# Kernel tuning notes

Hardware: AMD Instinct MI355X
Metric: run time of the kernel (lower is better)

Reference implementation:

```python
import jax, jax.numpy as jnp
import numpy as np

B, S, D = 2, 2048, 1024
E, K = 8, 2
CAP_FACTOR = 1.25
HID = 4 * D


def _capacity(num_tokens: int) -> int:
    import math
    cap = math.floor(K * CAP_FACTOR * num_tokens / E)
    cap += cap % 2
    return max(int(cap), 2)


def setup_inputs() -> dict:
    key = jax.random.key(0)
    k1, k2, k3, k4 = jax.random.split(key, 4)
    x = jax.random.normal(k1, (B, S, D), dtype=jnp.float32)
    w_gate = jax.random.normal(k2, (D, E), dtype=jnp.float32) * 0.02
    w_fc = jax.random.normal(k3, (E, D, HID), dtype=jnp.float32) * 0.02
    w_proj = jax.random.normal(k4, (E, HID, D), dtype=jnp.float32) * 0.02
    return {"x": x, "w_gate": w_gate, "w_fc": w_fc, "w_proj": w_proj}


def _moe_forward(x, w_gate, w_fc, w_proj):
    b, s, d = x.shape
    T = b * s
    cap = _capacity(T)
    xf = x.astype(jnp.float32).reshape(T, d)

    # --- Router (fp32, eval mode: no noise) ---
    logits = xf @ w_gate                                   # [T, E]
    top_v, top_i = jax.lax.top_k(logits, K)                # [T, K]
    NEG = jnp.float32(-1e30)
    masked = jnp.full_like(logits, NEG)
    masked = masked.at[jnp.arange(T)[:, None], top_i].set(top_v)
    probs = jax.nn.softmax(masked, axis=-1)                # [T, E], zero off top-k

    # --- Capacity assignment: cumsum over (k-major, token) flattened order ---
    oh = jax.nn.one_hot(top_i, E, dtype=jnp.int32)         # [T, K, E]
    oh = jnp.transpose(oh, (1, 0, 2))                      # [K, T, E]
    rank = jnp.cumsum(oh.reshape(K * T, E), axis=0).reshape(K, T, E) - 1
    within = (oh > 0) & (rank < cap)                       # [K, T, E]
    rank_sel = jnp.sum(jnp.where(within, rank, 0), axis=-1)  # [K, T]
    kept = jnp.any(within, axis=-1)                        # [K, T]

    p = jnp.take_along_axis(probs, top_i, axis=-1).T       # [K, T]
    w = jnp.where(kept, p, 0.0)                            # combine weights

    e_idx = top_i.T                                        # [K, T]
    t_idx = jnp.broadcast_to(jnp.arange(T)[None, :], (K, T))

    # expert_weights[t, e, c] (sparse scatter == torch one-hot combine)
    expert_weights = jnp.zeros((T, E, cap), jnp.float32)
    expert_weights = expert_weights.at[t_idx.ravel(), e_idx.ravel(), rank_sel.ravel()].add(w.ravel())

    # dispatch: expert_batches[e, c, :] = x of token routed to (e, c)
    disp = jnp.where(kept, 1.0, 0.0).ravel()[:, None]      # [K*T, 1]
    expert_batches = jnp.zeros((E, cap, d), jnp.float32)
    expert_batches = expert_batches.at[e_idx.ravel(), rank_sel.ravel()].add(disp * xf[t_idx.ravel()])

    # --- Expert MLPs (batched GEMMs, exact GELU, no bias, eval dropout) ---
    h = jnp.einsum('ecd,edh->ech', expert_batches, w_fc)
    h = jax.nn.gelu(h, approximate=False)
    expert_out = jnp.einsum('ech,ehd->ecd', h, w_proj)      # [E, cap, d]

    # --- Combine: gather expert outputs back to tokens weighted by router prob ---
    gathered = expert_out[e_idx.ravel(), rank_sel.ravel()].reshape(K, T, d)
    out_flat = jnp.sum(w[:, :, None] * gathered, axis=0)    # [T, d]
    output = out_flat.reshape(b, s, d)

    # --- Load balance loss (Switch) ---
    probs_full = jax.nn.softmax(logits, axis=-1)
    prob_per_expert = jnp.mean(probs_full, axis=0)          # [E]
    tokens_per_expert = jax.lax.stop_gradient(
        jnp.sum((expert_weights > 0).astype(jnp.float32), axis=(0, 2)) / (T * K)
    )
    lb_loss = E * jnp.sum(prob_per_expert * tokens_per_expert)

    # --- Router z-loss ---
    z_loss = jnp.mean(jax.nn.logsumexp(logits, axis=-1) ** 2)
    return output, lb_loss, z_loss


def reference(x, w_gate, w_fc, w_proj):
    return _moe_forward(x, w_gate, w_fc, w_proj)
```

## Files before the change

### kernel.cpp

```cpp
#include <hip/hip_runtime.h>
#include <hip/hip_bf16.h>
#include <cstdint>
#include <cstddef>

#define T_TOK 4096
#define D_DIM 1024
#define E_EXP 8
#define KSEL 2
#define CAP 1280
#define HID_DIM 4096

typedef __attribute__((ext_vector_type(8))) __bf16 bf16x8;
typedef __attribute__((ext_vector_type(8))) unsigned short ushort8;
typedef __attribute__((ext_vector_type(4))) float floatx4;

__device__ __forceinline__ unsigned short f2bf(float f) {
  unsigned int u = __builtin_bit_cast(unsigned int, f);
  u = (u + 0x7FFFu + ((u >> 16) & 1u)) >> 16;
  return (unsigned short)u;
}
__device__ __forceinline__ float bf2f(unsigned short h) {
  unsigned int u = ((unsigned int)h) << 16;
  return __builtin_bit_cast(float, u);
}

__device__ __forceinline__ void async16(const unsigned short* g, unsigned short* l) {
  __builtin_amdgcn_global_load_lds(
      (const __attribute__((address_space(1))) unsigned int*)g,
      (__attribute__((address_space(3))) unsigned int*)l, 16, 0, 0);
}

__global__ void router_kernel(const float* __restrict__ x, const float* __restrict__ wg,
                              int* __restrict__ top1, int* __restrict__ top2,
                              float* __restrict__ p0, float* __restrict__ p1,
                              float* __restrict__ probsum, float* __restrict__ zsum) {
  __shared__ float lps[E_EXP];
  __shared__ float lz;
  if (threadIdx.x < E_EXP) lps[threadIdx.x] = 0.f;
  if (threadIdx.x == 0) lz = 0.f;
  __syncthreads();
  int wave = threadIdx.x >> 6;
  int lane = threadIdx.x & 63;
  int t = blockIdx.x * 4 + wave;
  const float* xr = x + (size_t)t * D_DIM;
  float acc[E_EXP];
#pragma unroll
  for (int e = 0; e < E_EXP; ++e) acc[e] = 0.f;
  for (int j = 0; j < D_DIM / 64; ++j) {
    int i = lane + 64 * j;
    float xv = xr[i];
    const float4* wr = (const float4*)(wg + (size_t)i * E_EXP);
    float4 w0 = wr[0], w1 = wr[1];
    acc[0] += xv * w0.x; acc[1] += xv * w0.y; acc[2] += xv * w0.z; acc[3] += xv * w0.w;
    acc[4] += xv * w1.x; acc[5] += xv * w1.y; acc[6] += xv * w1.z; acc[7] += xv * w1.w;
  }
#pragma unroll
  for (int e = 0; e < E_EXP; ++e) {
#pragma unroll
    for (int s = 32; s > 0; s >>= 1) acc[e] += __shfl_xor(acc[e], s);
  }
  if (lane == 0) {
    int i1 = 0; float v1 = acc[0];
    for (int e = 1; e < E_EXP; ++e) if (acc[e] > v1) { v1 = acc[e]; i1 = e; }
    int i2 = -1; float v2 = -1e30f;
    for (int e = 0; e < E_EXP; ++e) if (e != i1 && acc[e] > v2) { v2 = acc[e]; i2 = e; }
    top1[t] = i1; top2[t] = i2;
    float dexp = expf(v2 - v1);
    p0[t] = 1.f / (1.f + dexp);
    p1[t] = dexp / (1.f + dexp);
    float pe[E_EXP]; float ssum = 0.f;
    for (int e = 0; e < E_EXP; ++e) { pe[e] = expf(acc[e] - v1); ssum += pe[e]; }
    float lse = logf(ssum) + v1;
    atomicAdd(&lz, lse * lse);
    float inv = 1.f / ssum;
    for (int e = 0; e < E_EXP; ++e) atomicAdd(&lps[e], pe[e] * inv);
  }
  __syncthreads();
  if (threadIdx.x < E_EXP) atomicAdd(&probsum[threadIdx.x], lps[threadIdx.x]);
  if (threadIdx.x == 0) atomicAdd(zsum, lz);
}

__global__ void scan_kernel(const int* __restrict__ top1, const int* __restrict__ top2,
                            int* __restrict__ rank0, int* __restrict__ rank1,
                            int* __restrict__ slot_token, int* __restrict__ cntk) {
  __shared__ int sc[256][E_EXP];
  int c = threadIdx.x;
  int e0l[16], e1l[16];
  int c0[E_EXP], c1[E_EXP];
#pragma unroll
  for (int e = 0; e < E_EXP; ++e) { c0[e] = 0; c1[e] = 0; }
#pragma unroll
  for (int j = 0; j < 16; ++j) {
    int t = c * 16 + j;
    int a = top1[t]; int b = top2[t];
    e0l[j] = a; e1l[j] = b;
    c0[a]++; c1[b]++;
  }
  for (int e = 0; e < E_EXP; ++e) sc[c][e] = c0[e];
  __syncthreads();
  for (int s = 1; s < 256; s <<= 1) {
    int tmp[E_EXP];
    if (c >= s) { for (int e = 0; e < E_EXP; ++e) tmp[e] = sc[c - s][e]; }
    __syncthreads();
    if (c >= s) { for (int e = 0; e < E_EXP; ++e) sc[c][e] += tmp[e]; }
    __syncthreads();
  }
  int off0[E_EXP], tot0[E_EXP];
  for (int e = 0; e < E_EXP; ++e) {
    off0[e] = (c > 0) ? sc[c - 1][e] : 0;
    tot0[e] = sc[255][e];
  }
  __syncthreads();
  for (int e = 0; e < E_EXP; ++e) sc[c][e] = c1[e];
  __syncthreads();
  for (int s = 1; s < 256; s <<= 1) {
    int tmp[E_EXP];
    if (c >= s) { for (int e = 0; e < E_EXP; ++e) tmp[e] = sc[c - s][e]; }
    __syncthreads();
    if (c >= s) { for (int e = 0; e < E_EXP; ++e) sc[c][e] += tmp[e]; }
    __syncthreads();
  }
  int off1[E_EXP], tot1[E_EXP];
  for (int e = 0; e < E_EXP; ++e) {
    off1[e] = (c > 0) ? sc[c - 1][e] : 0;
    tot1[e] = sc[255][e];
  }
  int run[E_EXP];
  for (int e = 0; e < E_EXP; ++e) run[e] = off0[e];
#pragma unroll
  for (int j = 0; j < 16; ++j) {
    int t = c * 16 + j;
    int e = e0l[j];
    int r = run[e]++;
    if (r < CAP) { rank0[t] = r; slot_token[e * CAP + r] = t; } else rank0[t] = -1;
  }
  for (int e = 0; e < E_EXP; ++e) run[e] = tot0[e] + off1[e];
#pragma unroll
  for (int j = 0; j < 16; ++j) {
    int t = c * 16 + j;
    int e = e1l[j];
    int r = run[e]++;
    if (r < CAP) { rank1[t] = r; slot_token[e * CAP + r] = t; } else rank1[t] = -1;
  }
  if (c == 0) {
    for (int e = 0; e < E_EXP; ++e) {
      int tot = tot0[e] + tot1[e];
      cntk[e] = tot < CAP ? tot : CAP;
    }
  }
}

__global__ void dispatch_kernel(const float* __restrict__ x, const int* __restrict__ slot_token,
                                unsigned short* __restrict__ batch) {
  int slot = blockIdx.x;
  int t = slot_token[slot];
  int d = threadIdx.x * 4;
  ushort4 o;
  if (t >= 0) {
    float4 v = *(const float4*)(x + (size_t)t * D_DIM + d);
    o.x = f2bf(v.x); o.y = f2bf(v.y); o.z = f2bf(v.z); o.w = f2bf(v.w);
  } else {
    o.x = 0; o.y = 0; o.z = 0; o.w = 0;
  }
  *(ushort4*)(batch + (size_t)slot * D_DIM + d) = o;
}

__global__ __launch_bounds__(256) void transpose_convert(const float* __restrict__ in,
                                                         unsigned short* __restrict__ out,
                                                         int R, int C) {
  __shared__ float tile[64][65];
  int b = blockIdx.z;
  int c0 = blockIdx.x * 64;
  int r0 = blockIdx.y * 64;
  const float* ip = in + (size_t)b * R * C;
  unsigned short* op = out + (size_t)b * R * C;
  int tid = threadIdx.x;
  int rr = tid >> 4;
  int cc = (tid & 15) * 4;
#pragma unroll
  for (int it = 0; it < 4; ++it) {
    int r = rr + it * 16;
    float4 v = *(const float4*)(ip + (size_t)(r0 + r) * C + c0 + cc);
    tile[r][cc] = v.x; tile[r][cc + 1] = v.y; tile[r][cc + 2] = v.z; tile[r][cc + 3] = v.w;
  }
  __syncthreads();
  int c = tid >> 2;
  int rq = (tid & 3) * 16;
  unsigned short vals[16];
#pragma unroll
  for (int j = 0; j < 16; ++j) vals[j] = f2bf(tile[rq + j][c]);
  unsigned short* dst = op + (size_t)(c0 + c) * R + r0 + rq;
  *(ushort8*)dst = *(ushort8*)&vals[0];
  *(ushort8*)(dst + 8) = *(ushort8*)&vals[8];
}

template <int KD, int NN, int NG_TILES, bool GELU>
__global__ __launch_bounds__(256) void gemm_alds(const unsigned short* __restrict__ A,
                                                 const unsigned short* __restrict__ BT,
                                                 unsigned short* __restrict__ Cd,
                                                 const int* __restrict__ cntk) {
  constexpr int MT = CAP / 128;
  constexpr int GRP = MT * NG_TILES;
  int bid = blockIdx.x;
  int e = bid & 7;
  int slot = bid >> 3;
  int ng = slot / GRP;
  int rem = slot - ng * GRP;
  int mm = rem / NG_TILES;
  int nw = rem - mm * NG_TILES;
  int m0 = mm * 128;
  int n0 = (ng * NG_TILES + nw) * 128;
  if (m0 >= cntk[e]) return;
  const unsigned short* Ae = A + (size_t)e * CAP * KD;
  const unsigned short* Be = BT + (size_t)e * NN * KD;
  unsigned short* Ce = Cd + (size_t)e * CAP * NN;
  __shared__ unsigned short As[128 * 32];
  __shared__ unsigned short Bs[128 * 32];
  int tid = threadIdx.x;
  int lane = tid & 63;
  int wv = tid >> 6;
  int wm = (wv & 1) * 64;
  int wn = (wv >> 1) * 64;
  int mrow = lane & 15;
  int kqb = lane >> 4;
  int sx = (mrow >> 1) & 3;
  int kb = (kqb ^ sx) * 8;
  floatx4 acc[4][4];
#pragma unroll
  for (int i = 0; i < 4; ++i)
#pragma unroll
    for (int j = 0; j < 4; ++j) {
      floatx4 z = {0.f, 0.f, 0.f, 0.f};
      acc[i][j] = z;
    }
  for (int k0 = 0; k0 < KD; k0 += 32) {
#pragma unroll
    for (int i = 0; i < 2; ++i) {
      int chw = i * 256 + wv * 64;
      int ch = chw + lane;
      int r = ch >> 2;
      int cbs = (ch & 3) ^ ((r >> 1) & 3);
      async16(&Ae[(size_t)(m0 + r) * KD + k0 + cbs * 8], &As[chw * 8]);
      async16(&Be[(size_t)(n0 + r) * KD + k0 + cbs * 8], &Bs[chw * 8]);
    }
    __syncthreads();
    bf16x8 af[4], bfr[4];
#pragma unroll
    for (int mt = 0; mt < 4; ++mt)
      af[mt] = *(const bf16x8*)(&As[(wm + mt * 16 + mrow) * 32 + kb]);
#pragma unroll
    for (int nt = 0; nt < 4; ++nt)
      bfr[nt] = *(const bf16x8*)(&Bs[(wn + nt * 16 + mrow) * 32 + kb]);
#pragma unroll
    for (int mt = 0; mt < 4; ++mt)
#pragma unroll
      for (int nt = 0; nt < 4; ++nt)
        acc[mt][nt] = __builtin_amdgcn_mfma_f32_16x16x32_bf16(af[mt], bfr[nt], acc[mt][nt], 0, 0, 0);
    __syncthreads();
  }
  int crow = (lane >> 4) * 4;
  int ccol = lane & 15;
#pragma unroll
  for (int mt = 0; mt < 4; ++mt)
#pragma unroll
    for (int nt = 0; nt < 4; ++nt)
#pragma unroll
      for (int r = 0; r < 4; ++r) {
        float v = acc[mt][nt][r];
        if (GELU) v = 0.5f * v * (1.f + erff(v * 0.70710678118654752f));
        Ce[(size_t)(m0 + wm + mt * 16 + crow + r) * NN + (n0 + wn + nt * 16 + ccol)] = f2bf(v);
      }
}

__global__ void combine_kernel(const unsigned short* __restrict__ EO,
                               const int* __restrict__ top1, const int* __restrict__ top2,
                               const float* __restrict__ p0, const float* __restrict__ p1,
                               const int* __restrict__ rank0, const int* __restrict__ rank1,
                               float* __restrict__ out) {
  int t = blockIdx.x;
  int d = threadIdx.x * 4;
  float a0 = 0.f, a1 = 0.f, a2 = 0.f, a3 = 0.f;
  int r0 = rank0[t];
  if (r0 >= 0) {
    float w = p0[t];
    ushort4 v = *(const ushort4*)(EO + ((size_t)top1[t] * CAP + r0) * D_DIM + d);
    a0 += w * bf2f(v.x); a1 += w * bf2f(v.y); a2 += w * bf2f(v.z); a3 += w * bf2f(v.w);
  }
  int r1 = rank1[t];
  if (r1 >= 0) {
    float w = p1[t];
    ushort4 v = *(const ushort4*)(EO + ((size_t)top2[t] * CAP + r1) * D_DIM + d);
    a0 += w * bf2f(v.x); a1 += w * bf2f(v.y); a2 += w * bf2f(v.z); a3 += w * bf2f(v.w);
  }
  float4 o; o.x = a0; o.y = a1; o.z = a2; o.w = a3;
  *(float4*)(out + (size_t)t * D_DIM + d) = o;
}

__global__ void finalize_kernel(const float* __restrict__ probsum, const float* __restrict__ zsum,
                                const int* __restrict__ cntk, float* __restrict__ out) {
  if (threadIdx.x == 0) {
    float lb = 0.f;
    for (int e = 0; e < E_EXP; ++e)
      lb += (probsum[e] / (float)T_TOK) * ((float)cntk[e] / (float)(T_TOK * KSEL));
    out[(size_t)T_TOK * D_DIM] = lb * (float)E_EXP;
    out[(size_t)T_TOK * D_DIM + 1] = zsum[0] / (float)T_TOK;
  }
}

extern "C" void kernel_launch(void* const* d_in, const int* in_sizes, int n_in,
                              void* d_out, int out_size, void* d_ws, size_t ws_size,
                              hipStream_t stream) {
  const float* x = (const float*)d_in[0];
  const float* w_gate = (const float*)d_in[1];
  const float* w_fc = (const float*)d_in[2];
  const float* w_proj = (const float*)d_in[3];
  float* out = (float*)d_out;
  char* ws = (char*)d_ws;

  float* probsum = (float*)(ws + 0);
  float* zsum    = (float*)(ws + 32);
  int*   cntk    = (int*)(ws + 64);
  int*   top1    = (int*)(ws + 4096);
  int*   top2    = (int*)(ws + 20480);
  float* p0      = (float*)(ws + 36864);
  float* p1      = (float*)(ws + 53248);
  int*   rank0   = (int*)(ws + 69632);
  int*   rank1   = (int*)(ws + 86016);
  int*   slot    = (int*)(ws + 102400);
  unsigned short* batch = (unsigned short*)(ws + 262144);
  unsigned short* H     = (unsigned short*)(ws + 262144 + 20971520);
  unsigned short* EO    = (unsigned short*)(ws + 262144 + 20971520 + 83886080);
  unsigned short* W     = (unsigned short*)(ws + 262144 + 20971520 + 83886080 + 20971520);

  hipMemsetAsync(ws, 0, 4096, stream);
  hipMemsetAsync(slot, 0xFF, E_EXP * CAP * sizeof(int), stream);

  router_kernel<<<T_TOK / 4, 256, 0, stream>>>(x, w_gate, top1, top2, p0, p1, probsum, zsum);
  scan_kernel<<<1, 256, 0, stream>>>(top1, top2, rank0, rank1, slot, cntk);
  dispatch_kernel<<<E_EXP * CAP, 256, 0, stream>>>(x, slot, batch);

  transpose_convert<<<dim3(HID_DIM / 64, D_DIM / 64, E_EXP), 256, 0, stream>>>(w_fc, W, D_DIM, HID_DIM);
  gemm_alds<D_DIM, HID_DIM, 4, true><<<8 * (HID_DIM / 128 / 4) * (CAP / 128) * 4, 256, 0, stream>>>(batch, W, H, cntk);

  transpose_convert<<<dim3(D_DIM / 64, HID_DIM / 64, E_EXP), 256, 0, stream>>>(w_proj, W, HID_DIM, D_DIM);
  gemm_alds<HID_DIM, D_DIM, 2, false><<<8 * (D_DIM / 128 / 2) * (CAP / 128) * 2, 256, 0, stream>>>(H, W, EO, cntk);

  combine_kernel<<<T_TOK, 256, 0, stream>>>(EO, top1, top2, p0, p1, rank0, rank1, out);
  finalize_kernel<<<1, 64, 0, stream>>>(probsum, zsum, cntk, out);
}
```

Before: 584.1 us.

## Fuse fp32 weight conversion and transpose into expert GEMM B-tile loads

Removes the separate transpose_convert passes that produced bf16 transposed weight copies, and instead has each GEMM block load fp32 weights directly, convert to bf16 in registers, and write a transposed tile into padded LDS. Also merges the finalize kernel into the combine kernel. This saves the extra weight read/write pass and two launches, but doubles per-block weight bytes fetched and replaces async global-to-LDS loads for B with synchronous loads, which may expose latency.

```diff
diff --git a/kernel.cpp b/kernel.cpp
--- a/kernel.cpp
+++ b/kernel.cpp
@@ -12,6 +12,7 @@
 
 typedef __attribute__((ext_vector_type(8))) __bf16 bf16x8;
 typedef __attribute__((ext_vector_type(8))) unsigned short ushort8;
+typedef __attribute__((ext_vector_type(4))) unsigned short ushort4v;
 typedef __attribute__((ext_vector_type(4))) float floatx4;
 
 __device__ __forceinline__ unsigned short f2bf(float f) {
@@ -165,40 +166,11 @@
   *(ushort4*)(batch + (size_t)slot * D_DIM + d) = o;
 }
 
-__global__ __launch_bounds__(256) void transpose_convert(const float* __restrict__ in,
-                                                         unsigned short* __restrict__ out,
-                                                         int R, int C) {
-  __shared__ float tile[64][65];
-  int b = blockIdx.z;
-  int c0 = blockIdx.x * 64;
-  int r0 = blockIdx.y * 64;
-  const float* ip = in + (size_t)b * R * C;
-  unsigned short* op = out + (size_t)b * R * C;
-  int tid = threadIdx.x;
-  int rr = tid >> 4;
-  int cc = (tid & 15) * 4;
-#pragma unroll
-  for (int it = 0; it < 4; ++it) {
-    int r = rr + it * 16;
-    float4 v = *(const float4*)(ip + (size_t)(r0 + r) * C + c0 + cc);
-    tile[r][cc] = v.x; tile[r][cc + 1] = v.y; tile[r][cc + 2] = v.z; tile[r][cc + 3] = v.w;
-  }
-  __syncthreads();
-  int c = tid >> 2;
-  int rq = (tid & 3) * 16;
-  unsigned short vals[16];
-#pragma unroll
-  for (int j = 0; j < 16; ++j) vals[j] = f2bf(tile[rq + j][c]);
-  unsigned short* dst = op + (size_t)(c0 + c) * R + r0 + rq;
-  *(ushort8*)dst = *(ushort8*)&vals[0];
-  *(ushort8*)(dst + 8) = *(ushort8*)&vals[8];
-}
-
 template <int KD, int NN, int NG_TILES, bool GELU>
-__global__ __launch_bounds__(256) void gemm_alds(const unsigned short* __restrict__ A,
-                                                 const unsigned short* __restrict__ BT,
-                                                 unsigned short* __restrict__ Cd,
-                                                 const int* __restrict__ cntk) {
+__global__ __launch_bounds__(256) void gemm_fwt(const unsigned short* __restrict__ A,
+                                                const float* __restrict__ W,
+                                                unsigned short* __restrict__ Cd,
+                                                const int* __restrict__ cntk) {
   constexpr int MT = CAP / 128;
   constexpr int GRP = MT * NG_TILES;
   int bid = blockIdx.x;
@@ -212,10 +184,10 @@
   int n0 = (ng * NG_TILES + nw) * 128;
   if (m0 >= cntk[e]) return;
   const unsigned short* Ae = A + (size_t)e * CAP * KD;
-  const unsigned short* Be = BT + (size_t)e * NN * KD;
+  const float* We = W + (size_t)e * KD * NN;
   unsigned short* Ce = Cd + (size_t)e * CAP * NN;
-  __shared__ unsigned short As[128 * 32];
-  __shared__ unsigned short Bs[128 * 32];
+  __shared__ __align__(16) unsigned short As[128 * 32];
+  __shared__ __align__(16) unsigned short Bs[128 * 72];
   int tid = threadIdx.x;
   int lane = tid & 63;
   int wv = tid >> 6;
@@ -225,6 +197,8 @@
   int kqb = lane >> 4;
   int sx = (mrow >> 1) & 3;
   int kb = (kqb ^ sx) * 8;
+  int bkm = tid & 7;
+  int bnm = tid >> 3;
   floatx4 acc[4][4];
 #pragma unroll
   for (int i = 0; i < 4; ++i)
@@ -241,7 +215,18 @@
       int r = ch >> 2;
       int cbs = (ch & 3) ^ ((r >> 1) & 3);
       async16(&Ae[(size_t)(m0 + r) * KD + k0 + cbs * 8], &As[chw * 8]);
-      async16(&Be[(size_t)(n0 + r) * KD + k0 + cbs * 8], &Bs[chw * 8]);
+    }
+    {
+      const float* wsrc = We + (size_t)(k0 + bkm * 4) * NN + n0 + bnm * 4;
+      unsigned short q[4][4];
+#pragma unroll
+      for (int j = 0; j < 4; ++j) {
+        float4 v = *(const float4*)(wsrc + (size_t)j * NN);
+        q[0][j] = f2bf(v.x); q[1][j] = f2bf(v.y); q[2][j] = f2bf(v.z); q[3][j] = f2bf(v.w);
+      }
+#pragma unroll
+      for (int jn = 0; jn < 4; ++jn)
+        *(ushort4v*)(&Bs[(bnm * 4 + jn) * 72 + bkm * 4]) = *(ushort4v*)&q[jn][0];
     }
     __syncthreads();
     bf16x8 af[4], bfr[4];
@@ -250,7 +235,7 @@
       af[mt] = *(const bf16x8*)(&As[(wm + mt * 16 + mrow) * 32 + kb]);
 #pragma unroll
     for (int nt = 0; nt < 4; ++nt)
-      bfr[nt] = *(const bf16x8*)(&Bs[(wn + nt * 16 + mrow) * 32 + kb]);
+      bfr[nt] = *(const bf16x8*)(&Bs[(wn + nt * 16 + mrow) * 72 + kqb * 8]);
 #pragma unroll
     for (int mt = 0; mt < 4; ++mt)
 #pragma unroll
@@ -276,7 +261,8 @@
                                const int* __restrict__ top1, const int* __restrict__ top2,
                                const float* __restrict__ p0, const float* __restrict__ p1,
                                const int* __restrict__ rank0, const int* __restrict__ rank1,
-                               float* __restrict__ out) {
+                               const float* __restrict__ probsum, const float* __restrict__ zsum,
+                               const int* __restrict__ cntk, float* __restrict__ out) {
   int t = blockIdx.x;
   int d = threadIdx.x * 4;
   float a0 = 0.f, a1 = 0.f, a2 = 0.f, a3 = 0.f;
@@ -294,11 +280,7 @@
   }
   float4 o; o.x = a0; o.y = a1; o.z = a2; o.w = a3;
   *(float4*)(out + (size_t)t * D_DIM + d) = o;
-}
-
-__global__ void finalize_kernel(const float* __restrict__ probsum, const float* __restrict__ zsum,
-                                const int* __restrict__ cntk, float* __restrict__ out) {
-  if (threadIdx.x == 0) {
+  if (t == 0 && threadIdx.x == 0) {
     float lb = 0.f;
     for (int e = 0; e < E_EXP; ++e)
       lb += (probsum[e] / (float)T_TOK) * ((float)cntk[e] / (float)(T_TOK * KSEL));
@@ -330,7 +312,6 @@
   unsigned short* batch = (unsigned short*)(ws + 262144);
   unsigned short* H     = (unsigned short*)(ws + 262144 + 20971520);
   unsigned short* EO    = (unsigned short*)(ws + 262144 + 20971520 + 83886080);
-  unsigned short* W     = (unsigned short*)(ws + 262144 + 20971520 + 83886080 + 20971520);
 
   hipMemsetAsync(ws, 0, 4096, stream);
   hipMemsetAsync(slot, 0xFF, E_EXP * CAP * sizeof(int), stream);
@@ -339,12 +320,10 @@
   scan_kernel<<<1, 256, 0, stream>>>(top1, top2, rank0, rank1, slot, cntk);
   dispatch_kernel<<<E_EXP * CAP, 256, 0, stream>>>(x, slot, batch);
 
-  transpose_convert<<<dim3(HID_DIM / 64, D_DIM / 64, E_EXP), 256, 0, stream>>>(w_fc, W, D_DIM, HID_DIM);
-  gemm_alds<D_DIM, HID_DIM, 4, true><<<8 * (HID_DIM / 128 / 4) * (CAP / 128) * 4, 256, 0, stream>>>(batch, W, H, cntk);
-
-  transpose_convert<<<dim3(D_DIM / 64, HID_DIM / 64, E_EXP), 256, 0, stream>>>(w_proj, W, HID_DIM, D_DIM);
-  gemm_alds<HID_DIM, D_DIM, 2, false><<<8 * (D_DIM / 128 / 2) * (CAP / 128) * 2, 256, 0, stream>>>(H, W, EO, cntk);
-
-  combine_kernel<<<T_TOK, 256, 0, stream>>>(EO, top1, top2, p0, p1, rank0, rank1, out);
-  finalize_kernel<<<1, 64, 0, stream>>>(probsum, zsum, cntk, out);
-}
+  gemm_fwt<D_DIM, HID_DIM, 4, true><<<8 * (HID_DIM / 128 / 4) * (CAP / 128) * 4, 256, 0, stream>>>(batch, w_fc, H, cntk);
+
+  gemm_fwt<HID_DIM, D_DIM, 2, false><<<8 * (D_DIM / 128 / 2) * (CAP / 128) * 2, 256, 0, stream>>>(H, w_proj, EO, cntk);
+
+  combine_kernel<<<T_TOK, 256, 0, stream>>>(EO, top1, top2, p0, p1, rank0, rank1,
+                                            probsum, zsum, cntk, out);
+}
```

Result: slower. 701.4 us (+20.1%).
